# Kernel optimization log

Measured on AMD Instinct MI355X. Metric: run time of the kernel, lower is better.

## Reference

```python
import jax, jax.numpy as jnp
import numpy as np

# Faithful JAX translation of fastmax_function with mask=True, p=1, normalize=0.
# In that branch the torch code sets temperature = 1 and uses a0 = a1 = 1.

def setup_inputs() -> dict:
    key = jax.random.key(0)
    kq, kk, kv = jax.random.split(key, 3)
    b, h, n, d = 2, 8, 8192, 32
    q = jax.random.normal(kq, (b, h, n, d), dtype=jnp.float32)
    k = jax.random.normal(kk, (b, h, n, d), dtype=jnp.float32)
    v = jax.random.normal(kv, (b, h, n, d), dtype=jnp.float32)
    return {"q": q, "k": k, "v": v}


def reference(q, k, v):
    # q, k, v: (b, h, n, d); causal (mask=True), p=1, a0=a1=1, temperature=1
    b, h, n, d = q.shape
    # first term: running sum of values
    first = jnp.cumsum(v, axis=2)                                  # (b,h,n,d)
    # second term: q_i . (sum_{j<=i} k_j v_j^T)
    kv = jnp.einsum('bhnd,bhne->bhnde', k, v)                      # (b,h,n,d,d)
    kv_cs = jnp.cumsum(kv, axis=2)                                 # (b,h,n,d,d)
    second = jnp.einsum('bhnd,bhnde->bhne', q, kv_cs)              # (b,h,n,d)
    # denominator: i + q_i . (sum_{j<=i} k_j)
    k_cs = jnp.cumsum(k, axis=2)                                   # (b,h,n,d)
    div1 = jnp.arange(1, n + 1, dtype=q.dtype)                     # (n,)
    div2 = jnp.einsum('bhnd,bhnd->bhn', q, k_cs)                   # (b,h,n)
    div = (div1[None, None, :] + div2)[..., None]                  # (b,h,n,1)
    return (first + second) / div
```

## Files before the change

kernel.cpp:

```cpp
#include <hip/hip_runtime.h>


#define D      32
#define C      64
#define NCHUNK 128
#define GSIZE  4
#define NGROUP 32
#define BH     16
#define NBLK   (BH * NCHUNK)
#define NGRP   (NBLK / GSIZE)
#define AGGU   1152

typedef __attribute__((ext_vector_type(8))) short bf16x8;
typedef __attribute__((ext_vector_type(4))) float f32x4;
typedef __attribute__((ext_vector_type(4))) unsigned short u16x4;

__device__ __forceinline__ unsigned short f2bf(float x) {
  union { float f; unsigned u; } c; c.f = x;
  unsigned r = (c.u + 0x7FFFu + ((c.u >> 16) & 1u)) >> 16;
  return (unsigned short)r;
}
__device__ __forceinline__ float bf2f(unsigned short u) {
  union { unsigned u; float f; } c; c.u = ((unsigned)u) << 16;
  return c.f;
}
__device__ __forceinline__ int permcol(int e) {
  return (e & 1) ? (16 + (e >> 1)) : (e >> 1);
}

__global__ __launch_bounds__(256) void state_scan_kernel(
    const float* __restrict__ k, const float* __restrict__ v,
    unsigned short* __restrict__ pref, unsigned short* __restrict__ gtot) {
  __shared__ __align__(16) unsigned short kT[D * 72];
  __shared__ __align__(16) unsigned short vT[D * 72];
  __shared__ __align__(16) float psK[1024];
  __shared__ __align__(16) float psV[1024];

  int t  = threadIdx.x;
  int j0 = t >> 3;
  int cb = (t & 7) * 4;
  int lane = t & 63, w = t >> 6;
  int m16 = lane & 15, quad = lane >> 4;
  int mb = w >> 1, nb = w & 1;
  int d1b = 16 * mb + quad * 4;
  int np  = permcol(16 * nb + m16);

  int c0 = blockIdx.x * GSIZE;
  const float4* kp = (const float4*)k + (size_t)c0 * 512;
  const float4* vp = (const float4*)v + (size_t)c0 * 512;

  float pr[4] = {0.f, 0.f, 0.f, 0.f};
  float tailpref = 0.f;

  float4 kA = kp[t], kB = kp[t + 256];
  float4 vA = vp[t], vB = vp[t + 256];

  for (int ci = 0; ci < GSIZE; ++ci) {
    {
      const float* ka = &kA.x; const float* kb = &kB.x;
      const float* va = &vA.x; const float* vb = &vB.x;
#pragma unroll
      for (int cc = 0; cc < 4; ++cc) {
        kT[(cb + cc) * 72 + j0]      = f2bf(ka[cc]);
        kT[(cb + cc) * 72 + j0 + 32] = f2bf(kb[cc]);
        vT[(cb + cc) * 72 + j0]      = f2bf(va[cc]);
        vT[(cb + cc) * 72 + j0 + 32] = f2bf(vb[cc]);
      }
      *(float4*)&psK[4 * t] =
          make_float4(kA.x + kB.x, kA.y + kB.y, kA.z + kB.z, kA.w + kB.w);
      *(float4*)&psV[4 * t] =
          make_float4(vA.x + vB.x, vA.y + vB.y, vA.z + vB.z, vA.w + vB.w);
    }
    __syncthreads();

    if (ci + 1 < GSIZE) {
      const float4* kn = kp + (size_t)(ci + 1) * 512;
      const float4* vn = vp + (size_t)(ci + 1) * 512;
      kA = kn[t]; kB = kn[t + 256];
      vA = vn[t]; vB = vn[t + 256];
    }

    f32x4 acc = {0.f, 0.f, 0.f, 0.f};
#pragma unroll
    for (int kb2 = 0; kb2 < 2; ++kb2) {
      bf16x8 a = *(const bf16x8*)&kT[(16 * mb + m16) * 72 + kb2 * 32 + quad * 8];
      bf16x8 b = *(const bf16x8*)&vT[(16 * nb + m16) * 72 + kb2 * 32 + quad * 8];
      acc = __builtin_amdgcn_mfma_f32_16x16x32_bf16(a, b, acc, 0, 0, 0);
    }
    float csum = 0.f;
    if (t < 64) {
      int ee = t & 31;
      const float* ps = (t < 32) ? psK : psV;
#pragma unroll
      for (int m = 0; m < 32; ++m) csum += ps[ee + 32 * m];
    }

    unsigned short* pc = pref + (size_t)(c0 + ci) * AGGU;
    *(u16x4*)&pc[np * 32 + d1b] =
        (u16x4){f2bf(pr[0]), f2bf(pr[1]), f2bf(pr[2]), f2bf(pr[3])};
#pragma unroll
    for (int reg = 0; reg < 4; ++reg) pr[reg] += acc[reg];
    if (t < 64) {
      ((float*)(pc + 1024))[t] = tailpref;
      tailpref += csum;
    }
    __syncthreads();
  }

  unsigned short* gt = gtot + (size_t)blockIdx.x * AGGU;
  *(u16x4*)&gt[np * 32 + d1b] =
      (u16x4){f2bf(pr[0]), f2bf(pr[1]), f2bf(pr[2]), f2bf(pr[3])};
  if (t < 64) ((float*)(gt + 1024))[t] = tailpref;
}

__global__ __launch_bounds__(256, 4) void output_kernel(
    const float* __restrict__ q, const float* __restrict__ k,
    const float* __restrict__ v, const unsigned short* __restrict__ pref,
    const unsigned short* __restrict__ gtot, float* __restrict__ out) {
  int g   = blockIdx.x & 31;
  int bh  = blockIdx.x >> 5;
  int blk0 = blockIdx.x * GSIZE;
  const float4* qp4 = (const float4*)q + (size_t)blk0 * 512;
  const float4* kp4 = (const float4*)k + (size_t)blk0 * 512;
  const float4* vp4 = (const float4*)v + (size_t)blk0 * 512;
  const unsigned short* prf = pref + (size_t)blk0 * AGGU;
  const unsigned short* gtb = gtot + (size_t)(bh * NGROUP) * AGGU;

  __shared__ __align__(16) char uA[10240];
  unsigned short* qbf = (unsigned short*)uA;
  unsigned short* kbf = (unsigned short*)(uA + 5120);
  float* q_s = (float*)uA;
  __shared__ __align__(16) unsigned short vTbf[D * 72];
  __shared__ __align__(16) unsigned short kvTbf[D * 40];
  __shared__ __align__(16) unsigned short Tbf[C * 72];
  __shared__ __align__(16) float kc_s[C * 36];
  __shared__ __align__(16) float gtot_s[8 * 32];
  __shared__ __align__(16) float pre_s[64];
  __shared__ __align__(16) float invdiv_s[C];

  int t  = threadIdx.x;
  int j0 = t >> 3;
  int cb = (t & 7) * 4;
  int lane = t & 63, w = t >> 6;
  int m16 = lane & 15, quad = lane >> 4;
  int rg = t >> 5;
  int e  = t & 31;

  float gs0 = 0.f, gs1 = 0.f, gs2 = 0.f, gs3 = 0.f, gtf = 0.f;
  for (int p0 = 0; p0 < g; p0 += 8) {
    uint2 r[8]; float tl[8];
#pragma unroll
    for (int u = 0; u < 8; ++u) {
      int p = p0 + u;
      const unsigned short* gp = gtb + (size_t)(p < g ? p : 0) * AGGU;
      r[u] = *(const uint2*)&gp[4 * t];
      if (t < 64) tl[u] = ((const float*)(gp + 1024))[t];
    }
#pragma unroll
    for (int u = 0; u < 8; ++u) {
      if (p0 + u < g) {
        gs0 += bf2f((unsigned short)(r[u].x & 0xffff));
        gs1 += bf2f((unsigned short)(r[u].x >> 16));
        gs2 += bf2f((unsigned short)(r[u].y & 0xffff));
        gs3 += bf2f((unsigned short)(r[u].y >> 16));
        if (t < 64) gtf += tl[u];
      }
    }
  }

  float4 qA = qp4[t], qB = qp4[t + 256];
  float4 kA = kp4[t], kB = kp4[t + 256];
  float4 vA = vp4[t], vB = vp4[t + 256];
  uint2 rp = *(const uint2*)&prf[4 * t];
  float tlp = (t < 64) ? ((const float*)(prf + 1024))[t] : 0.f;

  for (int ci = 0; ci < GSIZE; ++ci) {
    int blk = blk0 + ci;
    int c   = blk & 127;
    size_t off = (size_t)blk * (C * D);

    if (ci == 0) {
      for (int z = t; z < (C * 72) / 8; z += 256)
        ((uint4*)Tbf)[z] = make_uint4(0, 0, 0, 0);
    }

    *(float4*)&kc_s[j0 * 36 + cb]        = kA;
    *(float4*)&kc_s[(j0 + 32) * 36 + cb] = kB;
    *(u16x4*)&qbf[j0 * 40 + cb] =
        (u16x4){f2bf(qA.x), f2bf(qA.y), f2bf(qA.z), f2bf(qA.w)};
    *(u16x4*)&qbf[(j0 + 32) * 40 + cb] =
        (u16x4){f2bf(qB.x), f2bf(qB.y), f2bf(qB.z), f2bf(qB.w)};
    *(u16x4*)&kbf[j0 * 40 + cb] =
        (u16x4){f2bf(kA.x), f2bf(kA.y), f2bf(kA.z), f2bf(kA.w)};
    *(u16x4*)&kbf[(j0 + 32) * 40 + cb] =
        (u16x4){f2bf(kB.x), f2bf(kB.y), f2bf(kB.z), f2bf(kB.w)};
    {
      const float* va = &vA.x; const float* vb = &vB.x;
#pragma unroll
      for (int cc = 0; cc < 4; ++cc) {
        int n = permcol(cb + cc);
        vTbf[n * 72 + j0]      = f2bf(va[cc]);
        vTbf[n * 72 + j0 + 32] = f2bf(vb[cc]);
      }
    }
    {
      float s0 = gs0 + bf2f((unsigned short)(rp.x & 0xffff));
      float s1 = gs1 + bf2f((unsigned short)(rp.x >> 16));
      float s2 = gs2 + bf2f((unsigned short)(rp.y & 0xffff));
      float s3 = gs3 + bf2f((unsigned short)(rp.y >> 16));
      *(u16x4*)&kvTbf[(t >> 3) * 40 + (t & 7) * 4] =
          (u16x4){f2bf(s0), f2bf(s1), f2bf(s2), f2bf(s3)};
    }
    if (t < 64) pre_s[t] = gtf + tlp;
    __syncthreads();

    float4 nqA = make_float4(0,0,0,0), nqB = nqA, nkA = nqA, nkB = nqA,
           nvA = nqA, nvB = nqA;
    uint2 nrp = make_uint2(0, 0); float ntlp = 0.f;
    if (ci + 1 < GSIZE) {
      const float4* qn = qp4 + (size_t)(ci + 1) * 512;
      const float4* kn = kp4 + (size_t)(ci + 1) * 512;
      const float4* vn = vp4 + (size_t)(ci + 1) * 512;
      nqA = qn[t]; nqB = qn[t + 256];
      nkA = kn[t]; nkB = kn[t + 256];
      nvA = vn[t]; nvB = vn[t + 256];
      const unsigned short* pn = prf + (size_t)(ci + 1) * AGGU;
      nrp = *(const uint2*)&pn[4 * t];
      if (t < 64) ntlp = ((const float*)(pn + 1024))[t];
    }

    const bf16x8 aQ = *(const bf16x8*)&qbf[(16 * w + m16) * 40 + quad * 8];
    for (int jb = 0; jb <= w; ++jb) {
      bf16x8 bK = *(const bf16x8*)&kbf[(16 * jb + m16) * 40 + quad * 8];
      f32x4 cS = {0.f, 0.f, 0.f, 0.f};
      cS = __builtin_amdgcn_mfma_f32_16x16x32_bf16(aQ, bK, cS, 0, 0, 0);
      int jcol = 16 * jb + m16;
#pragma unroll
      for (int reg = 0; reg < 4; ++reg) {
        int i = 16 * w + quad * 4 + reg;
        float tv = (jcol <= i) ? (1.f + cS[reg]) : 0.f;
        Tbf[i * 72 + jcol] = f2bf(tv);
      }
    }
    float vals[8];
    {
      float run = 0.f;
#pragma unroll
      for (int r = 0; r < 8; ++r) {
        vals[r] = kc_s[(rg * 8 + r) * 36 + e];
        run += vals[r];
      }
      gtot_s[rg * 32 + e] = run;
    }
    __syncthreads();

    {
      float offv = pre_s[e];
      for (int g2 = 0; g2 < rg; ++g2) offv += gtot_s[g2 * 32 + e];
      float cacc = offv;
#pragma unroll
      for (int r = 0; r < 8; ++r) {
        cacc += vals[r];
        kc_s[(rg * 8 + r) * 36 + e] = cacc;
      }
    }
    *(float4*)&q_s[j0 * 36 + cb]        = qA;
    *(float4*)&q_s[(j0 + 32) * 36 + cb] = qB;
    __syncthreads();

    if (t < 64) {
      int i = t;
      float dp = 0.f;
#pragma unroll
      for (int d4 = 0; d4 < 8; ++d4) {
        float4 qv = *(const float4*)&q_s[i * 36 + 4 * d4];
        float4 kc = *(const float4*)&kc_s[i * 36 + 4 * d4];
        dp += qv.x * kc.x + qv.y * kc.y + qv.z * kc.z + qv.w * kc.w;
      }
      invdiv_s[i] = 1.f / ((float)(c * C + i + 1) + dp);
    }
    f32x4 o0 = {0.f, 0.f, 0.f, 0.f}, o1 = {0.f, 0.f, 0.f, 0.f};
    {
      bf16x8 b0 = *(const bf16x8*)&kvTbf[(m16)      * 40 + quad * 8];
      bf16x8 b1 = *(const bf16x8*)&kvTbf[(16 + m16) * 40 + quad * 8];
      o0 = __builtin_amdgcn_mfma_f32_16x16x32_bf16(aQ, b0, o0, 0, 0, 0);
      o1 = __builtin_amdgcn_mfma_f32_16x16x32_bf16(aQ, b1, o1, 0, 0, 0);
    }
    int kbcnt = (w >= 2) ? 2 : 1;
    for (int kb2 = 0; kb2 < kbcnt; ++kb2) {
      bf16x8 aT = *(const bf16x8*)&Tbf[(16 * w + m16) * 72 + kb2 * 32 + quad * 8];
      bf16x8 b0 = *(const bf16x8*)&vTbf[(m16)      * 72 + kb2 * 32 + quad * 8];
      bf16x8 b1 = *(const bf16x8*)&vTbf[(16 + m16) * 72 + kb2 * 32 + quad * 8];
      o0 = __builtin_amdgcn_mfma_f32_16x16x32_bf16(aT, b0, o0, 0, 0, 0);
      o1 = __builtin_amdgcn_mfma_f32_16x16x32_bf16(aT, b1, o1, 0, 0, 0);
    }
    __syncthreads();

    int e0 = 2 * m16;
#pragma unroll
    for (int reg = 0; reg < 4; ++reg) {
      int i = 16 * w + quad * 4 + reg;
      float id = invdiv_s[i];
      float2 o;
      o.x = (pre_s[32 + e0]     + o0[reg]) * id;
      o.y = (pre_s[32 + e0 + 1] + o1[reg]) * id;
      *(float2*)&out[off + (size_t)i * D + e0] = o;
    }
    __syncthreads();

    qA = nqA; qB = nqB; kA = nkA; kB = nkB; vA = nvA; vB = nvB;
    rp = nrp; tlp = ntlp;
  }
}

extern "C" void kernel_launch(void* const* d_in, const int* in_sizes, int n_in,
                              void* d_out, int out_size, void* d_ws, size_t ws_size,
                              hipStream_t stream) {
  const float* q = (const float*)d_in[0];
  const float* k = (const float*)d_in[1];
  const float* v = (const float*)d_in[2];
  float* out = (float*)d_out;
  unsigned short* pref = (unsigned short*)d_ws;
  unsigned short* gtot = pref + (size_t)NBLK * AGGU;

  state_scan_kernel<<<NGRP, 256, 0, stream>>>(k, v, pref, gtot);
  output_kernel<<<NGRP, 256, 0, stream>>>(q, k, v, pref, gtot, out);
}
```

Before: 103.6 us.

## Fuse state scan and output kernels with flag-based inter-block prefix handoff

Merges the two kernels into one. Each block computes its local KV and K-sum prefixes, keeps the per-chunk prefixes and the bf16 transposed V tiles in registers and shared memory, and publishes its group total to global memory with a flag. Later blocks in the same head spin on the flags of earlier groups before summing their totals. This drops the per-chunk prefix round trip through memory, the second read of k and v, and one kernel launch. In exchange it relies on all 512 blocks being co-resident to avoid deadlock, adds a bounded spin-wait and a memset launch, and raises shared memory use, which lowers occupancy.

Measured after the change: 158.6 us. 53.2% more time.

```diff
diff --git a/kernel.cpp b/kernel.cpp
--- a/kernel.cpp
+++ b/kernel.cpp
@@ -28,13 +28,25 @@
   return (e & 1) ? (16 + (e >> 1)) : (e >> 1);
 }
 
-__global__ __launch_bounds__(256) void state_scan_kernel(
-    const float* __restrict__ k, const float* __restrict__ v,
-    unsigned short* __restrict__ pref, unsigned short* __restrict__ gtot) {
-  __shared__ __align__(16) unsigned short kT[D * 72];
-  __shared__ __align__(16) unsigned short vT[D * 72];
-  __shared__ __align__(16) float psK[1024];
-  __shared__ __align__(16) float psV[1024];
+__global__ __launch_bounds__(256, 2) void fused_kernel(
+    const float* __restrict__ q, const float* __restrict__ k,
+    const float* __restrict__ v, unsigned short* __restrict__ gtot,
+    unsigned int* __restrict__ flags, float* __restrict__ out) {
+  __shared__ __align__(16) char smem[51200];
+  unsigned short* vT4 = (unsigned short*)smem;
+  char* arena = smem + 18432;
+  unsigned short* kT  = (unsigned short*)arena;
+  float* psK = (float*)(arena + 4608);
+  float* psV = (float*)(arena + 8704);
+  unsigned short* qbf = (unsigned short*)arena;
+  unsigned short* kbf = (unsigned short*)(arena + 5120);
+  float* q_s = (float*)arena;
+  unsigned short* kvTbf = (unsigned short*)(arena + 10240);
+  unsigned short* Tbf   = (unsigned short*)(arena + 12800);
+  float* kc_s   = (float*)(arena + 22016);
+  float* gtot_s = (float*)(arena + 31232);
+  float* pre_s  = (float*)(arena + 32256);
+  float* invdiv_s = (float*)(arena + 32512);
 
   int t  = threadIdx.x;
   int j0 = t >> 3;
@@ -44,47 +56,62 @@
   int mb = w >> 1, nb = w & 1;
   int d1b = 16 * mb + quad * 4;
   int np  = permcol(16 * nb + m16);
-
-  int c0 = blockIdx.x * GSIZE;
-  const float4* kp = (const float4*)k + (size_t)c0 * 512;
-  const float4* vp = (const float4*)v + (size_t)c0 * 512;
-
-  float pr[4] = {0.f, 0.f, 0.f, 0.f};
-  float tailpref = 0.f;
-
-  float4 kA = kp[t], kB = kp[t + 256];
+  int rg  = t >> 5;
+  int e   = t & 31;
+  int g   = blockIdx.x & (NGROUP - 1);
+  int bh  = blockIdx.x >> 5;
+  int blk0 = blockIdx.x * GSIZE;
+  int myoff = np * 32 + d1b;
+
+  const float4* kp  = (const float4*)k + (size_t)blk0 * 512;
+  const float4* vp  = (const float4*)v + (size_t)blk0 * 512;
+  const float4* qp4 = (const float4*)q + (size_t)blk0 * 512;
+  const unsigned short* gtb = gtot + (size_t)(bh * NGROUP) * AGGU;
+
+  for (int z = t; z < (C * 72) / 8; z += 256)
+    ((uint4*)Tbf)[z] = make_uint4(0, 0, 0, 0);
+
+  float4 kHA[4], kHB[4];
+  float prefs[4][4], tails[4];
+  float pr0 = 0.f, pr1 = 0.f, pr2 = 0.f, pr3 = 0.f, tailpref = 0.f;
+
+  kHA[0] = kp[t]; kHB[0] = kp[t + 256];
   float4 vA = vp[t], vB = vp[t + 256];
 
+#pragma unroll
   for (int ci = 0; ci < GSIZE; ++ci) {
-    {
-      const float* ka = &kA.x; const float* kb = &kB.x;
-      const float* va = &vA.x; const float* vb = &vB.x;
+    unsigned short* vTc = vT4 + ci * (D * 72);
+    {
+      const float* ka = &kHA[ci].x; const float* kb = &kHB[ci].x;
+      const float* va = &vA.x;      const float* vb = &vB.x;
 #pragma unroll
       for (int cc = 0; cc < 4; ++cc) {
         kT[(cb + cc) * 72 + j0]      = f2bf(ka[cc]);
         kT[(cb + cc) * 72 + j0 + 32] = f2bf(kb[cc]);
-        vT[(cb + cc) * 72 + j0]      = f2bf(va[cc]);
-        vT[(cb + cc) * 72 + j0 + 32] = f2bf(vb[cc]);
-      }
-      *(float4*)&psK[4 * t] =
-          make_float4(kA.x + kB.x, kA.y + kB.y, kA.z + kB.z, kA.w + kB.w);
+        int n = permcol(cb + cc);
+        vTc[n * 72 + j0]      = f2bf(va[cc]);
+        vTc[n * 72 + j0 + 32] = f2bf(vb[cc]);
+      }
+      *(float4*)&psK[4 * t] = make_float4(kHA[ci].x + kHB[ci].x,
+                                          kHA[ci].y + kHB[ci].y,
+                                          kHA[ci].z + kHB[ci].z,
+                                          kHA[ci].w + kHB[ci].w);
       *(float4*)&psV[4 * t] =
           make_float4(vA.x + vB.x, vA.y + vB.y, vA.z + vB.z, vA.w + vB.w);
     }
     __syncthreads();
 
     if (ci + 1 < GSIZE) {
-      const float4* kn = kp + (size_t)(ci + 1) * 512;
-      const float4* vn = vp + (size_t)(ci + 1) * 512;
-      kA = kn[t]; kB = kn[t + 256];
-      vA = vn[t]; vB = vn[t + 256];
+      kHA[ci + 1] = kp[(ci + 1) * 512 + t];
+      kHB[ci + 1] = kp[(ci + 1) * 512 + t + 256];
+      vA = vp[(ci + 1) * 512 + t]; vB = vp[(ci + 1) * 512 + t + 256];
     }
 
     f32x4 acc = {0.f, 0.f, 0.f, 0.f};
 #pragma unroll
     for (int kb2 = 0; kb2 < 2; ++kb2) {
       bf16x8 a = *(const bf16x8*)&kT[(16 * mb + m16) * 72 + kb2 * 32 + quad * 8];
-      bf16x8 b = *(const bf16x8*)&vT[(16 * nb + m16) * 72 + kb2 * 32 + quad * 8];
+      bf16x8 b = *(const bf16x8*)&vTc[np * 72 + kb2 * 32 + quad * 8];
       acc = __builtin_amdgcn_mfma_f32_16x16x32_bf16(a, b, acc, 0, 0, 0);
     }
     float csum = 0.f;
@@ -94,57 +121,37 @@
 #pragma unroll
       for (int m = 0; m < 32; ++m) csum += ps[ee + 32 * m];
     }
-
-    unsigned short* pc = pref + (size_t)(c0 + ci) * AGGU;
-    *(u16x4*)&pc[np * 32 + d1b] =
-        (u16x4){f2bf(pr[0]), f2bf(pr[1]), f2bf(pr[2]), f2bf(pr[3])};
-#pragma unroll
-    for (int reg = 0; reg < 4; ++reg) pr[reg] += acc[reg];
-    if (t < 64) {
-      ((float*)(pc + 1024))[t] = tailpref;
-      tailpref += csum;
-    }
-    __syncthreads();
-  }
-
-  unsigned short* gt = gtot + (size_t)blockIdx.x * AGGU;
-  *(u16x4*)&gt[np * 32 + d1b] =
-      (u16x4){f2bf(pr[0]), f2bf(pr[1]), f2bf(pr[2]), f2bf(pr[3])};
-  if (t < 64) ((float*)(gt + 1024))[t] = tailpref;
-}
-
-__global__ __launch_bounds__(256, 4) void output_kernel(
-    const float* __restrict__ q, const float* __restrict__ k,
-    const float* __restrict__ v, const unsigned short* __restrict__ pref,
-    const unsigned short* __restrict__ gtot, float* __restrict__ out) {
-  int g   = blockIdx.x & 31;
-  int bh  = blockIdx.x >> 5;
-  int blk0 = blockIdx.x * GSIZE;
-  const float4* qp4 = (const float4*)q + (size_t)blk0 * 512;
-  const float4* kp4 = (const float4*)k + (size_t)blk0 * 512;
-  const float4* vp4 = (const float4*)v + (size_t)blk0 * 512;
-  const unsigned short* prf = pref + (size_t)blk0 * AGGU;
-  const unsigned short* gtb = gtot + (size_t)(bh * NGROUP) * AGGU;
-
-  __shared__ __align__(16) char uA[10240];
-  unsigned short* qbf = (unsigned short*)uA;
-  unsigned short* kbf = (unsigned short*)(uA + 5120);
-  float* q_s = (float*)uA;
-  __shared__ __align__(16) unsigned short vTbf[D * 72];
-  __shared__ __align__(16) unsigned short kvTbf[D * 40];
-  __shared__ __align__(16) unsigned short Tbf[C * 72];
-  __shared__ __align__(16) float kc_s[C * 36];
-  __shared__ __align__(16) float gtot_s[8 * 32];
-  __shared__ __align__(16) float pre_s[64];
-  __shared__ __align__(16) float invdiv_s[C];
-
-  int t  = threadIdx.x;
-  int j0 = t >> 3;
-  int cb = (t & 7) * 4;
-  int lane = t & 63, w = t >> 6;
-  int m16 = lane & 15, quad = lane >> 4;
-  int rg = t >> 5;
-  int e  = t & 31;
+    prefs[ci][0] = pr0; prefs[ci][1] = pr1;
+    prefs[ci][2] = pr2; prefs[ci][3] = pr3;
+    tails[ci] = tailpref;
+    pr0 += acc[0]; pr1 += acc[1]; pr2 += acc[2]; pr3 += acc[3];
+    tailpref += csum;
+    __syncthreads();
+  }
+
+  {
+    unsigned short* gt = gtot + (size_t)blockIdx.x * AGGU;
+    *(u16x4*)&gt[myoff] =
+        (u16x4){f2bf(pr0), f2bf(pr1), f2bf(pr2), f2bf(pr3)};
+    if (t < 64) ((float*)(gt + 1024))[t] = tailpref;
+  }
+  __syncthreads();
+  if (t == 0) {
+    __threadfence();
+    atomicExch(&flags[blockIdx.x], 1u);
+  }
+
+  float4 qA = qp4[t], qB = qp4[t + 256];
+
+  if (t < g) {
+    int guard = 0;
+    while (atomicAdd(&flags[(bh << 5) + t], 0u) == 0u && guard < (1 << 22)) {
+      __builtin_amdgcn_s_sleep(2);
+      ++guard;
+    }
+  }
+  __syncthreads();
+  __threadfence();
 
   float gs0 = 0.f, gs1 = 0.f, gs2 = 0.f, gs3 = 0.f, gtf = 0.f;
   for (int p0 = 0; p0 < g; p0 += 8) {
@@ -153,7 +160,7 @@
     for (int u = 0; u < 8; ++u) {
       int p = p0 + u;
       const unsigned short* gp = gtb + (size_t)(p < g ? p : 0) * AGGU;
-      r[u] = *(const uint2*)&gp[4 * t];
+      r[u] = *(const uint2*)&gp[myoff];
       if (t < 64) tl[u] = ((const float*)(gp + 1024))[t];
     }
 #pragma unroll
@@ -168,65 +175,40 @@
     }
   }
 
-  float4 qA = qp4[t], qB = qp4[t + 256];
-  float4 kA = kp4[t], kB = kp4[t + 256];
-  float4 vA = vp4[t], vB = vp4[t + 256];
-  uint2 rp = *(const uint2*)&prf[4 * t];
-  float tlp = (t < 64) ? ((const float*)(prf + 1024))[t] : 0.f;
-
+#pragma unroll
   for (int ci = 0; ci < GSIZE; ++ci) {
     int blk = blk0 + ci;
     int c   = blk & 127;
     size_t off = (size_t)blk * (C * D);
-
-    if (ci == 0) {
-      for (int z = t; z < (C * 72) / 8; z += 256)
-        ((uint4*)Tbf)[z] = make_uint4(0, 0, 0, 0);
-    }
-
-    *(float4*)&kc_s[j0 * 36 + cb]        = kA;
-    *(float4*)&kc_s[(j0 + 32) * 36 + cb] = kB;
+    const unsigned short* vTc = vT4 + ci * (D * 72);
+
+    *(float4*)&kc_s[j0 * 36 + cb]        = kHA[ci];
+    *(float4*)&kc_s[(j0 + 32) * 36 + cb] = kHB[ci];
     *(u16x4*)&qbf[j0 * 40 + cb] =
         (u16x4){f2bf(qA.x), f2bf(qA.y), f2bf(qA.z), f2bf(qA.w)};
     *(u16x4*)&qbf[(j0 + 32) * 40 + cb] =
         (u16x4){f2bf(qB.x), f2bf(qB.y), f2bf(qB.z), f2bf(qB.w)};
     *(u16x4*)&kbf[j0 * 40 + cb] =
-        (u16x4){f2bf(kA.x), f2bf(kA.y), f2bf(kA.z), f2bf(kA.w)};
+        (u16x4){f2bf(kHA[ci].x), f2bf(kHA[ci].y),
+                f2bf(kHA[ci].z), f2bf(kHA[ci].w)};
     *(u16x4*)&kbf[(j0 + 32) * 40 + cb] =
-        (u16x4){f2bf(kB.x), f2bf(kB.y), f2bf(kB.z), f2bf(kB.w)};
-    {
-      const float* va = &vA.x; const float* vb = &vB.x;
-#pragma unroll
-      for (int cc = 0; cc < 4; ++cc) {
-        int n = permcol(cb + cc);
-        vTbf[n * 72 + j0]      = f2bf(va[cc]);
-        vTbf[n * 72 + j0 + 32] = f2bf(vb[cc]);
-      }
-    }
-    {
-      float s0 = gs0 + bf2f((unsigned short)(rp.x & 0xffff));
-      float s1 = gs1 + bf2f((unsigned short)(rp.x >> 16));
-      float s2 = gs2 + bf2f((unsigned short)(rp.y & 0xffff));
-      float s3 = gs3 + bf2f((unsigned short)(rp.y >> 16));
-      *(u16x4*)&kvTbf[(t >> 3) * 40 + (t & 7) * 4] =
+        (u16x4){f2bf(kHB[ci].x), f2bf(kHB[ci].y),
+                f2bf(kHB[ci].z), f2bf(kHB[ci].w)};
+    {
+      float s0 = gs0 + prefs[ci][0];
+      float s1 = gs1 + prefs[ci][1];
+      float s2 = gs2 + prefs[ci][2];
+      float s3 = gs3 + prefs[ci][3];
+      *(u16x4*)&kvTbf[np * 40 + d1b] =
           (u16x4){f2bf(s0), f2bf(s1), f2bf(s2), f2bf(s3)};
     }
-    if (t < 64) pre_s[t] = gtf + tlp;
-    __syncthreads();
-
-    float4 nqA = make_float4(0,0,0,0), nqB = nqA, nkA = nqA, nkB = nqA,
-           nvA = nqA, nvB = nqA;
-    uint2 nrp = make_uint2(0, 0); float ntlp = 0.f;
+    if (t < 64) pre_s[t] = gtf + tails[ci];
+    __syncthreads();
+
+    float4 nqA = make_float4(0, 0, 0, 0), nqB = nqA;
     if (ci + 1 < GSIZE) {
-      const float4* qn = qp4 + (size_t)(ci + 1) * 512;
-      const float4* kn = kp4 + (size_t)(ci + 1) * 512;
-      const float4* vn = vp4 + (size_t)(ci + 1) * 512;
-      nqA = qn[t]; nqB = qn[t + 256];
-      nkA = kn[t]; nkB = kn[t + 256];
-      nvA = vn[t]; nvB = vn[t + 256];
-      const unsigned short* pn = prf + (size_t)(ci + 1) * AGGU;
-      nrp = *(const uint2*)&pn[4 * t];
-      if (t < 64) ntlp = ((const float*)(pn + 1024))[t];
+      nqA = qp4[(ci + 1) * 512 + t];
+      nqB = qp4[(ci + 1) * 512 + t + 256];
     }
 
     const bf16x8 aQ = *(const bf16x8*)&qbf[(16 * w + m16) * 40 + quad * 8];
@@ -289,8 +271,8 @@
     int kbcnt = (w >= 2) ? 2 : 1;
     for (int kb2 = 0; kb2 < kbcnt; ++kb2) {
       bf16x8 aT = *(const bf16x8*)&Tbf[(16 * w + m16) * 72 + kb2 * 32 + quad * 8];
-      bf16x8 b0 = *(const bf16x8*)&vTbf[(m16)      * 72 + kb2 * 32 + quad * 8];
-      bf16x8 b1 = *(const bf16x8*)&vTbf[(16 + m16) * 72 + kb2 * 32 + quad * 8];
+      bf16x8 b0 = *(const bf16x8*)&vTc[(m16)      * 72 + kb2 * 32 + quad * 8];
+      bf16x8 b1 = *(const bf16x8*)&vTc[(16 + m16) * 72 + kb2 * 32 + quad * 8];
       o0 = __builtin_amdgcn_mfma_f32_16x16x32_bf16(aT, b0, o0, 0, 0, 0);
       o1 = __builtin_amdgcn_mfma_f32_16x16x32_bf16(aT, b1, o1, 0, 0, 0);
     }
@@ -308,8 +290,7 @@
     }
     __syncthreads();
 
-    qA = nqA; qB = nqB; kA = nkA; kB = nkB; vA = nvA; vB = nvB;
-    rp = nrp; tlp = ntlp;
+    qA = nqA; qB = nqB;
   }
 }
 
@@ -320,9 +301,10 @@
   const float* k = (const float*)d_in[1];
   const float* v = (const float*)d_in[2];
   float* out = (float*)d_out;
-  unsigned short* pref = (unsigned short*)d_ws;
-  unsigned short* gtot = pref + (size_t)NBLK * AGGU;
-
-  state_scan_kernel<<<NGRP, 256, 0, stream>>>(k, v, pref, gtot);
-  output_kernel<<<NGRP, 256, 0, stream>>>(q, k, v, pref, gtot, out);
-}
+  unsigned short* gtot = (unsigned short*)d_ws;
+  unsigned int* flags =
+      (unsigned int*)((char*)d_ws + (size_t)NGRP * AGGU * 2);
+
+  hipMemsetAsync(flags, 0, NGRP * sizeof(unsigned int), stream);
+  fused_kernel<<<NGRP, 256, 0, stream>>>(q, k, v, gtot, flags, out);
+}
```
